# Performance work log

Hardware: AMD Instinct MI355X
Metric: run time of the kernel (lower is better)

The kernel has to match this reference:

```python
import jax, jax.numpy as jnp
import numpy as np

IMG = 144      # image height/width
P = 4          # patch size
NP = IMG // P  # patches per side (36)
N = NP * NP * (IMG // NP // P if False else 1) * (IMG * IMG // (P * P) // (NP * NP))  # placeholder
N = IMG * IMG // (P * P)  # 1296 tokens (C=1)
E = P * P      # embedding dim = 16


def setup_inputs() -> dict:
    key = jax.random.key(0)
    x = jax.random.uniform(key, (4, 1, IMG, IMG), dtype=jnp.float32)
    return {"x": x}


def reference(x) -> jnp.ndarray:
    B = x.shape[0]
    x_max = jnp.max(x)
    xn = x / x_max

    # SimplePatching: img.unfold(3,P,P).unfold(4,P,P).reshape(B,-1,P*P)
    # For C=1 this flattening is exactly row-major reshape: each token is a
    # 1xP^2 horizontal strip of pixels.
    tkn = xn.reshape(B, N, E)  # (B, N, E)

    # SimpleMSA with n_heads=1 (forced by the repeat/view), scale=1.0:
    # attn[b,i,j] = softmax_j( -mean_d (t_i - t_j)^2 )
    diff = tkn[:, :, None, :] - tkn[:, None, :, :]        # (B, N, N, E)
    d2 = jnp.mean(jnp.square(diff), axis=-1)              # (B, N, N)
    attn = jax.nn.softmax(-d2, axis=-1)                   # (B, N, N)
    out = jnp.einsum('bij,bjd->bid', attn, tkn)           # (B, N, E)

    # SimpleMerging: view(B,1,N,P^2) -> permute -> view(B,P^2,N) -> F.fold
    # fold with kernel=stride=P is a pure permutation reshape:
    # out_img[b, by*P+ky, bx*P+kx] = m[b, ky*P+kx, by*NP+bx]
    m = out.transpose(0, 2, 1)                            # (B, P^2, N)
    m = m.reshape(B, P, P, NP, NP)                        # (B, ky, kx, by, bx)
    img = m.transpose(0, 3, 1, 4, 2).reshape(B, 1, IMG, IMG)
    return img * x_max
```

## Files before the change

kernel.cpp:

```cpp
#include <hip/hip_runtime.h>

#define IMGX   144
#define PATCH  4
#define NPS    36
#define NTOKB  1296
#define ED     16
#define NTOK   5184
#define RPW    4
#define BPB    324
#define NCHUNK 21
#define PREP_BLOCKS 21

__device__ float  g_partial[PREP_BLOCKS];
__device__ float  g_norms[NTOK];
__device__ float2 g_xt[4 * 8 * NTOKB];

__global__ __launch_bounds__(256) void prep_kernel(const float* __restrict__ x) {
    __shared__ float wmax[4];
    const int tid = threadIdx.x;
    const int t = blockIdx.x * 256 + tid;
    float m = 0.0f;
    if (t < NTOK) {
        const float4* p = (const float4*)(x + t * ED);
        float4 a = p[0], bq = p[1], cq = p[2], dq = p[3];
        float ns = 0.0f;
        ns = fmaf(a.x, a.x, ns);   ns = fmaf(a.y, a.y, ns);
        ns = fmaf(a.z, a.z, ns);   ns = fmaf(a.w, a.w, ns);
        ns = fmaf(bq.x, bq.x, ns); ns = fmaf(bq.y, bq.y, ns);
        ns = fmaf(bq.z, bq.z, ns); ns = fmaf(bq.w, bq.w, ns);
        ns = fmaf(cq.x, cq.x, ns); ns = fmaf(cq.y, cq.y, ns);
        ns = fmaf(cq.z, cq.z, ns); ns = fmaf(cq.w, cq.w, ns);
        ns = fmaf(dq.x, dq.x, ns); ns = fmaf(dq.y, dq.y, ns);
        ns = fmaf(dq.z, dq.z, ns); ns = fmaf(dq.w, dq.w, ns);
        g_norms[t] = ns;

        const int bb = t / NTOKB;
        const int jb = t - bb * NTOKB;
        float2* xt = g_xt + bb * (8 * NTOKB) + jb;
        xt[0 * NTOKB] = make_float2(a.x, a.y);
        xt[1 * NTOKB] = make_float2(a.z, a.w);
        xt[2 * NTOKB] = make_float2(bq.x, bq.y);
        xt[3 * NTOKB] = make_float2(bq.z, bq.w);
        xt[4 * NTOKB] = make_float2(cq.x, cq.y);
        xt[5 * NTOKB] = make_float2(cq.z, cq.w);
        xt[6 * NTOKB] = make_float2(dq.x, dq.y);
        xt[7 * NTOKB] = make_float2(dq.z, dq.w);

        m = fmaxf(fmaxf(fmaxf(a.x, a.y), fmaxf(a.z, a.w)),
                  fmaxf(fmaxf(fmaxf(bq.x, bq.y), fmaxf(bq.z, bq.w)),
                        fmaxf(fmaxf(fmaxf(cq.x, cq.y), fmaxf(cq.z, cq.w)),
                              fmaxf(fmaxf(dq.x, dq.y), fmaxf(dq.z, dq.w)))));
    }
#pragma unroll
    for (int s = 32; s; s >>= 1) m = fmaxf(m, __shfl_xor(m, s));
    if ((tid & 63) == 0) wmax[tid >> 6] = m;
    __syncthreads();
    if (tid == 0) {
        g_partial[blockIdx.x] = fmaxf(fmaxf(wmax[0], wmax[1]), fmaxf(wmax[2], wmax[3]));
    }
}

__global__ __launch_bounds__(256, 2) void attn_kernel(const float* __restrict__ x,
                                                      float* __restrict__ out) {
    __shared__ float redo[4][64];
    __shared__ float redd[4][4];

    const int tid  = threadIdx.x;
    const int lane = tid & 63;
    const int w    = tid >> 6;
    const int blk  = blockIdx.x;
    const int b    = blk / BPB;
    const int i0   = (blk - b * BPB) * RPW;

    const float*  __restrict__ xb    = x + b * (NTOKB * ED);
    const float*  __restrict__ norms = g_norms + b * NTOKB;
    const float2* __restrict__ xt    = g_xt + b * (8 * NTOKB);

    float pm = (lane < PREP_BLOCKS) ? g_partial[lane] : 0.0f;
#pragma unroll
    for (int sh = 32; sh; sh >>= 1) pm = fmaxf(pm, __shfl_xor(pm, sh));
    const float xmax = pm;
    const float s  = 1.0f / (16.0f * xmax * xmax);
    const float c2 = 2.0f * s * 1.4426950408889634f;
    const float cf = s * 1.4426950408889634f;

    float2 ti[4][8];
#pragma unroll
    for (int r = 0; r < 4; r++) {
        const float4* p = (const float4*)(xb + (i0 + r) * ED);
#pragma unroll
        for (int q = 0; q < 4; q++) {
            const float4 a = p[q];
            ti[r][2 * q + 0] = make_float2(a.x * c2, a.y * c2);
            ti[r][2 * q + 1] = make_float2(a.z * c2, a.w * c2);
        }
    }

    float2 o[4][8];
#pragma unroll
    for (int r = 0; r < 4; r++)
#pragma unroll
        for (int h = 0; h < 8; h++) { o[r][h].x = 0.f; o[r][h].y = 0.f; }
    float den0 = 0.f, den1 = 0.f, den2 = 0.f, den3 = 0.f;

    float2 cur[8];
    float  njc;
    {
        const int j = w * 64 + lane;
#pragma unroll
        for (int h = 0; h < 8; h++) cur[h] = xt[h * NTOKB + j];
        njc = norms[j];
    }

    for (int t = 0; ; t++) {
        const int c    = w + 4 * t;
        const int cnx  = c + 4;
        const bool more = (cnx < NCHUNK);

        float2 nxt[8];
        float  njn = 0.f;
        if (more) {
            const int j  = cnx * 64 + lane;
            const int jc = (j < NTOKB) ? j : 0;
#pragma unroll
            for (int h = 0; h < 8; h++) nxt[h] = xt[h * NTOKB + jc];
            njn = norms[jc];
        }

        const bool valid = (c * 64 + lane) < NTOKB;

        float d0 = 0.f, d1 = 0.f, d2 = 0.f, d3 = 0.f;
#pragma unroll
        for (int h = 0; h < 8; h++) {
            const float2 t2 = cur[h];
            d0 = fmaf(ti[0][h].x, t2.x, d0); d0 = fmaf(ti[0][h].y, t2.y, d0);
            d1 = fmaf(ti[1][h].x, t2.x, d1); d1 = fmaf(ti[1][h].y, t2.y, d1);
            d2 = fmaf(ti[2][h].x, t2.x, d2); d2 = fmaf(ti[2][h].y, t2.y, d2);
            d3 = fmaf(ti[3][h].x, t2.x, d3); d3 = fmaf(ti[3][h].y, t2.y, d3);
        }

        const float cc = cf * njc;
        float e0 = __builtin_amdgcn_exp2f(d0 - cc);
        float e1 = __builtin_amdgcn_exp2f(d1 - cc);
        float e2 = __builtin_amdgcn_exp2f(d2 - cc);
        float e3 = __builtin_amdgcn_exp2f(d3 - cc);
        e0 = valid ? e0 : 0.f;
        e1 = valid ? e1 : 0.f;
        e2 = valid ? e2 : 0.f;
        e3 = valid ? e3 : 0.f;
        den0 += e0; den1 += e1; den2 += e2; den3 += e3;
#pragma unroll
        for (int h = 0; h < 8; h++) {
            const float2 t2 = cur[h];
            o[0][h].x = fmaf(e0, t2.x, o[0][h].x); o[0][h].y = fmaf(e0, t2.y, o[0][h].y);
            o[1][h].x = fmaf(e1, t2.x, o[1][h].x); o[1][h].y = fmaf(e1, t2.y, o[1][h].y);
            o[2][h].x = fmaf(e2, t2.x, o[2][h].x); o[2][h].y = fmaf(e2, t2.y, o[2][h].y);
            o[3][h].x = fmaf(e3, t2.x, o[3][h].x); o[3][h].y = fmaf(e3, t2.y, o[3][h].y);
        }

        if (!more) break;
#pragma unroll
        for (int h = 0; h < 8; h++) cur[h] = nxt[h];
        njc = njn;
    }

#pragma unroll
    for (int sh = 32; sh; sh >>= 1) {
        den0 += __shfl_xor(den0, sh);
        den1 += __shfl_xor(den1, sh);
        den2 += __shfl_xor(den2, sh);
        den3 += __shfl_xor(den3, sh);
    }

#define CMP2(v, c) ((c) ? (v).y : (v).x)
#define V(n) CMP2(o[(n) >> 4][((n) >> 1) & 7], (n) & 1)
#define BSTAGE(M)                                                   \
    {                                                               \
        const bool hi = (lane & (M)) != 0;                          \
        _Pragma("unroll")                                           \
        for (int k = 0; k < (M); k++) {                             \
            const float give = hi ? V(k) : V(k + (M));              \
            const float got  = __shfl_xor(give, (M));               \
            V(k) = (hi ? V(k + (M)) : V(k)) + got;                  \
        }                                                           \
    }
    BSTAGE(32) BSTAGE(16) BSTAGE(8) BSTAGE(4) BSTAGE(2) BSTAGE(1)

    redo[w][lane] = V(0);
    if (lane == 0) {
        redd[w][0] = den0; redd[w][1] = den1; redd[w][2] = den2; redd[w][3] = den3;
    }
    __syncthreads();

    if (w == 0) {
        const float v = redo[0][lane] + redo[1][lane] + redo[2][lane] + redo[3][lane];
        const int r = lane >> 4;
        const int d = lane & 15;
        const float den = redd[0][r] + redd[1][r] + redd[2][r] + redd[3][r];
        const float val = v / den;

        const int i  = i0 + r;
        const int by = i / NPS;
        const int bx = i - by * NPS;
        out[b * (IMGX * IMGX) + (by * PATCH + (d >> 2)) * IMGX + bx * PATCH + (d & 3)] = val;
    }
#undef V
#undef CMP2
#undef BSTAGE
}

extern "C" void kernel_launch(void* const* d_in, const int* in_sizes, int n_in,
                              void* d_out, int out_size, void* d_ws, size_t ws_size,
                              hipStream_t stream) {
    const float* x = (const float*)d_in[0];
    float* out = (float*)d_out;
    (void)d_ws; (void)ws_size;

    hipLaunchKernelGGL(prep_kernel, dim3(PREP_BLOCKS), dim3(256), 0, stream, x);
    hipLaunchKernelGGL(attn_kernel, dim3(NTOKB), dim3(256), 0, stream, x, out);
}
```

Baseline: 75.33 us.

## Pad key tokens to fixed length and fully unroll double-buffered chunk loop

Result: no change. 74.24 us (-1.4%).

```diff
diff --git a/kernel.cpp b/kernel.cpp
--- a/kernel.cpp
+++ b/kernel.cpp
@@ -4,16 +4,16 @@
 #define PATCH  4
 #define NPS    36
 #define NTOKB  1296
+#define NTP    1536
 #define ED     16
 #define NTOK   5184
 #define RPW    4
 #define BPB    324
-#define NCHUNK 21
-#define PREP_BLOCKS 21
+#define PREP_BLOCKS 24
 
 __device__ float  g_partial[PREP_BLOCKS];
-__device__ float  g_norms[NTOK];
-__device__ float2 g_xt[4 * 8 * NTOKB];
+__device__ float  g_norms[4 * NTP];
+__device__ float2 g_xt[4 * 8 * NTP];
 
 __global__ __launch_bounds__(256) void prep_kernel(const float* __restrict__ x) {
     __shared__ float wmax[4];
@@ -32,24 +32,33 @@
         ns = fmaf(cq.z, cq.z, ns); ns = fmaf(cq.w, cq.w, ns);
         ns = fmaf(dq.x, dq.x, ns); ns = fmaf(dq.y, dq.y, ns);
         ns = fmaf(dq.z, dq.z, ns); ns = fmaf(dq.w, dq.w, ns);
-        g_norms[t] = ns;
 
         const int bb = t / NTOKB;
         const int jb = t - bb * NTOKB;
-        float2* xt = g_xt + bb * (8 * NTOKB) + jb;
-        xt[0 * NTOKB] = make_float2(a.x, a.y);
-        xt[1 * NTOKB] = make_float2(a.z, a.w);
-        xt[2 * NTOKB] = make_float2(bq.x, bq.y);
-        xt[3 * NTOKB] = make_float2(bq.z, bq.w);
-        xt[4 * NTOKB] = make_float2(cq.x, cq.y);
-        xt[5 * NTOKB] = make_float2(cq.z, cq.w);
-        xt[6 * NTOKB] = make_float2(dq.x, dq.y);
-        xt[7 * NTOKB] = make_float2(dq.z, dq.w);
+        g_norms[bb * NTP + jb] = ns;
+        float2* xt = g_xt + bb * (8 * NTP) + jb;
+        xt[0 * NTP] = make_float2(a.x, a.y);
+        xt[1 * NTP] = make_float2(a.z, a.w);
+        xt[2 * NTP] = make_float2(bq.x, bq.y);
+        xt[3 * NTP] = make_float2(bq.z, bq.w);
+        xt[4 * NTP] = make_float2(cq.x, cq.y);
+        xt[5 * NTP] = make_float2(cq.z, cq.w);
+        xt[6 * NTP] = make_float2(dq.x, dq.y);
+        xt[7 * NTP] = make_float2(dq.z, dq.w);
 
         m = fmaxf(fmaxf(fmaxf(a.x, a.y), fmaxf(a.z, a.w)),
                   fmaxf(fmaxf(fmaxf(bq.x, bq.y), fmaxf(bq.z, bq.w)),
                         fmaxf(fmaxf(fmaxf(cq.x, cq.y), fmaxf(cq.z, cq.w)),
                               fmaxf(fmaxf(dq.x, dq.y), fmaxf(dq.z, dq.w)))));
+    } else {
+        const int p  = t - NTOK;
+        const int bb = p / 240;
+        const int jb = NTOKB + (p - bb * 240);
+        g_norms[bb * NTP + jb] = 1.0e9f;
+        float2* xt = g_xt + bb * (8 * NTP) + jb;
+        const float2 z = make_float2(0.f, 0.f);
+        xt[0 * NTP] = z; xt[1 * NTP] = z; xt[2 * NTP] = z; xt[3 * NTP] = z;
+        xt[4 * NTP] = z; xt[5 * NTP] = z; xt[6 * NTP] = z; xt[7 * NTP] = z;
     }
 #pragma unroll
     for (int s = 32; s; s >>= 1) m = fmaxf(m, __shfl_xor(m, s));
@@ -60,8 +69,9 @@
     }
 }
 
-__global__ __launch_bounds__(256, 2) void attn_kernel(const float* __restrict__ x,
-                                                      float* __restrict__ out) {
+__global__ __attribute__((amdgpu_waves_per_eu(2, 2)))
+__launch_bounds__(256) void attn_kernel(const float* __restrict__ x,
+                                        float* __restrict__ out) {
     __shared__ float redo[4][64];
     __shared__ float redd[4][4];
 
@@ -72,9 +82,9 @@
     const int b    = blk / BPB;
     const int i0   = (blk - b * BPB) * RPW;
 
-    const float*  __restrict__ xb    = x + b * (NTOKB * ED);
-    const float*  __restrict__ norms = g_norms + b * NTOKB;
-    const float2* __restrict__ xt    = g_xt + b * (8 * NTOKB);
+    const float*  __restrict__ xb = x + b * (NTOKB * ED);
+    const float2* __restrict__ xw = g_xt + b * (8 * NTP) + (w * 64 + lane);
+    const float*  __restrict__ nr = g_norms + b * NTP + (w * 64 + lane);
 
     float pm = (lane < PREP_BLOCKS) ? g_partial[lane] : 0.0f;
 #pragma unroll
@@ -103,66 +113,57 @@
         for (int h = 0; h < 8; h++) { o[r][h].x = 0.f; o[r][h].y = 0.f; }
     float den0 = 0.f, den1 = 0.f, den2 = 0.f, den3 = 0.f;
 
-    float2 cur[8];
-    float  njc;
-    {
-        const int j = w * 64 + lane;
-#pragma unroll
-        for (int h = 0; h < 8; h++) cur[h] = xt[h * NTOKB + j];
-        njc = norms[j];
-    }
-
-    for (int t = 0; ; t++) {
-        const int c    = w + 4 * t;
-        const int cnx  = c + 4;
-        const bool more = (cnx < NCHUNK);
-
-        float2 nxt[8];
-        float  njn = 0.f;
-        if (more) {
-            const int j  = cnx * 64 + lane;
-            const int jc = (j < NTOKB) ? j : 0;
-#pragma unroll
-            for (int h = 0; h < 8; h++) nxt[h] = xt[h * NTOKB + jc];
-            njn = norms[jc];
-        }
-
-        const bool valid = (c * 64 + lane) < NTOKB;
-
-        float d0 = 0.f, d1 = 0.f, d2 = 0.f, d3 = 0.f;
-#pragma unroll
-        for (int h = 0; h < 8; h++) {
-            const float2 t2 = cur[h];
-            d0 = fmaf(ti[0][h].x, t2.x, d0); d0 = fmaf(ti[0][h].y, t2.y, d0);
-            d1 = fmaf(ti[1][h].x, t2.x, d1); d1 = fmaf(ti[1][h].y, t2.y, d1);
-            d2 = fmaf(ti[2][h].x, t2.x, d2); d2 = fmaf(ti[2][h].y, t2.y, d2);
-            d3 = fmaf(ti[3][h].x, t2.x, d3); d3 = fmaf(ti[3][h].y, t2.y, d3);
-        }
-
-        const float cc = cf * njc;
-        float e0 = __builtin_amdgcn_exp2f(d0 - cc);
-        float e1 = __builtin_amdgcn_exp2f(d1 - cc);
-        float e2 = __builtin_amdgcn_exp2f(d2 - cc);
-        float e3 = __builtin_amdgcn_exp2f(d3 - cc);
-        e0 = valid ? e0 : 0.f;
-        e1 = valid ? e1 : 0.f;
-        e2 = valid ? e2 : 0.f;
-        e3 = valid ? e3 : 0.f;
-        den0 += e0; den1 += e1; den2 += e2; den3 += e3;
-#pragma unroll
-        for (int h = 0; h < 8; h++) {
-            const float2 t2 = cur[h];
-            o[0][h].x = fmaf(e0, t2.x, o[0][h].x); o[0][h].y = fmaf(e0, t2.y, o[0][h].y);
-            o[1][h].x = fmaf(e1, t2.x, o[1][h].x); o[1][h].y = fmaf(e1, t2.y, o[1][h].y);
-            o[2][h].x = fmaf(e2, t2.x, o[2][h].x); o[2][h].y = fmaf(e2, t2.y, o[2][h].y);
-            o[3][h].x = fmaf(e3, t2.x, o[3][h].x); o[3][h].y = fmaf(e3, t2.y, o[3][h].y);
-        }
-
-        if (!more) break;
-#pragma unroll
-        for (int h = 0; h < 8; h++) cur[h] = nxt[h];
-        njc = njn;
-    }
+    float2 bkA[8], bkB[8];
+    float  njA, njB;
+
+#define LOADX(BK, NJ, T)                                                 \
+    {                                                                    \
+        _Pragma("unroll")                                                \
+        for (int h = 0; h < 8; h++) BK[h] = xw[h * NTP + 256 * (T)];     \
+        NJ = nr[256 * (T)];                                              \
+    }
+
+#define CHUNK(BK, NJ)                                                            \
+    {                                                                            \
+        float d0 = 0.f, d1 = 0.f, d2 = 0.f, d3 = 0.f;                            \
+        _Pragma("unroll")                                                        \
+        for (int h = 0; h < 8; h++) {                                            \
+            const float2 t2 = BK[h];                                             \
+            d0 = fmaf(ti[0][h].x, t2.x, d0); d0 = fmaf(ti[0][h].y, t2.y, d0);    \
+            d1 = fmaf(ti[1][h].x, t2.x, d1); d1 = fmaf(ti[1][h].y, t2.y, d1);    \
+            d2 = fmaf(ti[2][h].x, t2.x, d2); d2 = fmaf(ti[2][h].y, t2.y, d2);    \
+            d3 = fmaf(ti[3][h].x, t2.x, d3); d3 = fmaf(ti[3][h].y, t2.y, d3);    \
+        }                                                                        \
+        const float cc = cf * (NJ);                                              \
+        const float e0 = __builtin_amdgcn_exp2f(d0 - cc);                        \
+        const float e1 = __builtin_amdgcn_exp2f(d1 - cc);                        \
+        const float e2 = __builtin_amdgcn_exp2f(d2 - cc);                        \
+        const float e3 = __builtin_amdgcn_exp2f(d3 - cc);                        \
+        den0 += e0; den1 += e1; den2 += e2; den3 += e3;                          \
+        _Pragma("unroll")                                                        \
+        for (int h = 0; h < 8; h++) {                                            \
+            const float2 t2 = BK[h];                                             \
+            o[0][h].x = fmaf(e0, t2.x, o[0][h].x); o[0][h].y = fmaf(e0, t2.y, o[0][h].y); \
+            o[1][h].x = fmaf(e1, t2.x, o[1][h].x); o[1][h].y = fmaf(e1, t2.y, o[1][h].y); \
+            o[2][h].x = fmaf(e2, t2.x, o[2][h].x); o[2][h].y = fmaf(e2, t2.y, o[2][h].y); \
+            o[3][h].x = fmaf(e3, t2.x, o[3][h].x); o[3][h].y = fmaf(e3, t2.y, o[3][h].y); \
+        }                                                                        \
+    }
+
+    LOADX(bkA, njA, 0)
+    LOADX(bkB, njB, 1)
+    CHUNK(bkA, njA)
+    LOADX(bkA, njA, 2)
+    CHUNK(bkB, njB)
+    LOADX(bkB, njB, 3)
+    CHUNK(bkA, njA)
+    LOADX(bkA, njA, 4)
+    CHUNK(bkB, njB)
+    LOADX(bkB, njB, 5)
+    CHUNK(bkA, njA)
+    CHUNK(bkB, njB)
+#undef LOADX
+#undef CHUNK
 
 #pragma unroll
     for (int sh = 32; sh; sh >>= 1) {
```
